# Optimization experiments

Measured on AMD Instinct MI355X. Metric: run time of the kernel, lower is better.

## Reference

```python
import jax, jax.numpy as jnp
import numpy as np

EMBED_DIM = 512
B, N = 8, 2048


def setup_inputs() -> dict:
    key = jax.random.key(0)
    ks = jax.random.split(key, 9)
    d = EMBED_DIM
    s = 1.0 / np.sqrt(d)
    return {
        "x": jax.random.normal(ks[0], (B, N, d), dtype=jnp.float32),
        "Wq": jax.random.uniform(ks[1], (d, d), jnp.float32, -s, s),
        "bq": jax.random.uniform(ks[2], (d,), jnp.float32, -s, s),
        "Wk": jax.random.uniform(ks[3], (d, d), jnp.float32, -s, s),
        "bk": jax.random.uniform(ks[4], (d,), jnp.float32, -s, s),
        "Wv": jax.random.uniform(ks[5], (d, d), jnp.float32, -s, s),
        "bv": jax.random.uniform(ks[6], (d,), jnp.float32, -s, s),
        "Wo": jax.random.uniform(ks[7], (d, d), jnp.float32, -s, s),
        "bo": jax.random.uniform(ks[8], (d,), jnp.float32, -s, s),
    }


def reference(x, Wq, bq, Wk, bk, Wv, bv, Wo, bo):
    d = x.shape[-1]
    scale = d ** (-0.5)
    q = x @ Wq + bq              # [B, N, D]
    k = x @ Wk + bk
    v = x @ Wv + bv
    attn = jnp.einsum('bnd,bmd->bnm', q, k) * scale  # [B, N, N]
    attn = jax.nn.softmax(attn, axis=-1)
    out = jnp.einsum('bnm,bmd->bnd', attn, v)
    return out @ Wo + bo
```

## Files before the change

kernel.cpp:

```cpp
#include <hip/hip_runtime.h>
#include <hip/hip_bf16.h>
#include <hip/hip_fp8.h>
#include <stdint.h>

typedef __bf16 bf16;
typedef __attribute__((ext_vector_type(8))) short short8;
typedef __attribute__((ext_vector_type(4))) float f32x4;
typedef __attribute__((ext_vector_type(4))) bf16 bf16x4;
typedef __attribute__((ext_vector_type(8))) int int8v;
typedef __attribute__((ext_vector_type(4))) int int4v;

#define DIM 512
#define NBATCH 8
#define SEQ 2048

#define VMCNT(N) asm volatile("s_waitcnt vmcnt(" #N ")" ::: "memory")
#define LGKMCNT0 asm volatile("s_waitcnt lgkmcnt(0)" ::: "memory")
#define CFENCE   asm volatile("" ::: "memory")

__device__ __forceinline__ void gld_lds16(const void* g, void* l) {
    __builtin_amdgcn_global_load_lds(
        (const __attribute__((address_space(1))) void*)g,
        (__attribute__((address_space(3))) void*)l,
        16, 0, 0);
}

__device__ __forceinline__ unsigned char f32_to_e4m3(float v) {
#if __has_builtin(__builtin_amdgcn_cvt_pk_fp8_f32)
    return (unsigned char)(__builtin_amdgcn_cvt_pk_fp8_f32(v, v, 0, false) & 0xff);
#else
    return __hip_cvt_float_to_fp8(v, __HIP_SATFINITE, __HIP_E4M3);
#endif
}

template <int MODE, int SWIZ>
__global__ __launch_bounds__(256) void gemm_bt(
    const bf16* __restrict__ A, const bf16* __restrict__ Bt,
    void* __restrict__ Cv, uint8_t* __restrict__ Vt,
    const float* __restrict__ bias, int N, int K, int gx)
{
    __shared__ bf16 smem[32768];
    bf16* Asb = smem;
    bf16* Bsb = smem + 16384;

    int bx, by;
    {
        const unsigned g = blockIdx.x;
        const unsigned xcd = g & 7;
        const unsigned t = g >> 3;
        const unsigned per = (gridDim.x >> 3) / (unsigned)gx;
        by = xcd * per + t / (unsigned)gx;
        bx = t % (unsigned)gx;
    }

    const int tid  = threadIdx.x;
    const int lane = tid & 63;
    const int w    = tid >> 6;
    const int wr   = w >> 1;
    const int wc   = w & 1;
    const int lm   = lane & 15;
    const int lk   = lane >> 4;
    const int fs   = lm & 7;
    const int rq   = tid >> 3;
    const int pc   = tid & 7;
    const int scol = ((pc ^ (rq & 7)) * 8);

    const bf16* Ag = A + (size_t)(by * 128) * K;
    const bf16* Bg = Bt + (size_t)(bx * 128) * K;

    f32x4 acc[4][4];
#pragma unroll
    for (int i = 0; i < 4; ++i)
#pragma unroll
        for (int j = 0; j < 4; ++j)
            acc[i][j] = (f32x4){0.f, 0.f, 0.f, 0.f};

    auto stage = [&](int kb, int buf) {
#pragma unroll
        for (int t = 0; t < 4; ++t) {
            const int r = t * 32 + rq;
            gld_lds16(Ag + (size_t)r * K + kb + scol,
                      Asb + buf * 8192 + t * 2048 + tid * 8);
            gld_lds16(Bg + (size_t)r * K + kb + scol,
                      Bsb + buf * 8192 + t * 2048 + tid * 8);
        }
    };
    auto compute = [&](int buf) {
        const bf16* Ab = Asb + buf * 8192;
        const bf16* Bb = Bsb + buf * 8192;
#pragma unroll
        for (int s = 0; s < 2; ++s) {
            const int u = ((s * 4 + lk) ^ fs) * 8;
            short8 fa[4], fb[4];
#pragma unroll
            for (int i = 0; i < 4; ++i)
                fa[i] = *(const short8*)&Ab[(wr * 64 + i * 16 + lm) * 64 + u];
#pragma unroll
            for (int j = 0; j < 4; ++j)
                fb[j] = *(const short8*)&Bb[(wc * 64 + j * 16 + lm) * 64 + u];
#pragma unroll
            for (int i = 0; i < 4; ++i)
#pragma unroll
                for (int j = 0; j < 4; ++j)
                    acc[i][j] = __builtin_amdgcn_mfma_f32_16x16x32_bf16(
                        fa[i], fb[j], acc[i][j], 0, 0, 0);
        }
    };

    stage(0, 0);
    const int E = K >> 6;
#pragma unroll 2
    for (int e = 0; e < E; ++e) {
        const int p = e & 1;
        CFENCE;
        __builtin_amdgcn_s_barrier();
        CFENCE;
        if (e + 1 < E) { stage((e + 1) << 6, p ^ 1); VMCNT(8); }
        else           { VMCNT(0); }
        CFENCE;
        __builtin_amdgcn_s_barrier();
        CFENCE;
        __builtin_amdgcn_s_setprio(1);
        compute(p);
        __builtin_amdgcn_s_setprio(0);
    }
    __syncthreads();

#pragma unroll
    for (int i = 0; i < 4; ++i)
#pragma unroll
        for (int j = 0; j < 4; ++j) {
            const int col = bx * 128 + wc * 64 + j * 16 + lm;
            const float bv = bias[col];
#pragma unroll
            for (int r = 0; r < 4; ++r)
                acc[i][j][r] += bv;
        }

    if (MODE == 2) {
        float* ft = (float*)smem;
        float* outp = (float*)Cv;
#pragma unroll
        for (int h = 0; h < 2; ++h) {
            if (wr == h) {
#pragma unroll
                for (int i = 0; i < 4; ++i)
#pragma unroll
                    for (int j = 0; j < 4; ++j)
#pragma unroll
                        for (int r = 0; r < 4; ++r)
                            ft[(i * 16 + lk * 4 + r) * 132 + wc * 64 + j * 16 + lm] =
                                acc[i][j][r];
            }
            __syncthreads();
            const int rr = tid >> 5, cc = (tid & 31) * 4;
#pragma unroll
            for (int p = 0; p < 8; ++p) {
                const int row = p * 8 + rr;
                *(float4*)&outp[(size_t)(by * 128 + h * 64 + row) * N +
                                bx * 128 + cc] = *(const float4*)&ft[row * 132 + cc];
            }
            __syncthreads();
        }
        return;
    }

    const int sub  = (bx * 128) >> 9;
    const int col0 = (bx * 128) & 511;

    if (sub == 2) {
        const int b  = (by * 128) >> 11;
        const int n0 = (by * 128) & 2047;
        uint8_t* t8 = (uint8_t*)smem;
#pragma unroll
        for (int i = 0; i < 4; ++i)
#pragma unroll
            for (int j = 0; j < 4; ++j)
#pragma unroll
                for (int r = 0; r < 4; ++r) {
                    const int fl = wc * 64 + j * 16 + lm;
                    const int nl = wr * 64 + i * 16 + lk * 4 + r;
                    t8[fl * 144 + nl] = f32_to_e4m3(32.0f * acc[i][j][r]);
                }
        __syncthreads();
        const int f = tid >> 1, nh = (tid & 1) * 64;
#pragma unroll
        for (int p = 0; p < 4; ++p) {
            const uint4 raw = *(const uint4*)&t8[f * 144 + nh + p * 16];
            *(uint4*)&Vt[((size_t)(b * 512 + col0 + f)) * 2048 +
                         n0 + nh + p * 16] = raw;
        }
        return;
    }

    uint8_t* d8 = (uint8_t*)Cv + (size_t)sub * 8388608;
    uint8_t* t8 = (uint8_t*)smem;
#pragma unroll
    for (int h = 0; h < 2; ++h) {
        if (wr == h) {
#pragma unroll
            for (int i = 0; i < 4; ++i)
#pragma unroll
                for (int j = 0; j < 4; ++j)
#pragma unroll
                    for (int r = 0; r < 4; ++r)
                        t8[(i * 16 + lk * 4 + r) * 144 + wc * 64 + j * 16 + lm] =
                            f32_to_e4m3(32.0f * acc[i][j][r]);
        }
        __syncthreads();
        const int rr = tid >> 3, cc = (tid & 7) * 16;
#pragma unroll
        for (int p = 0; p < 2; ++p) {
            const int row = p * 32 + rr;
            const uint4 raw = *(const uint4*)&t8[row * 144 + cc];
            *(uint4*)&d8[(size_t)(by * 128 + h * 64 + row) * 512 + col0 + cc] =
                raw;
        }
        __syncthreads();
    }
}

template <int MODE, int E>
__global__ __launch_bounds__(256) void gemm_mx(
    const uint8_t* __restrict__ A, const uint8_t* __restrict__ Bt,
    void* __restrict__ Cv, float* __restrict__ rsum,
    int N, int K, long long sA, long long sB, long long sC, float alpha,
    int gx)
{
    __shared__ uint8_t smem[49152];
    uint8_t* Ab  = smem;
    uint8_t* Bsb = smem + 16384;

    int bx, by, bz;
    {
        const unsigned g = blockIdx.x;
        bz = g & 7;
        const unsigned r = g >> 3;
        bx = r % (unsigned)gx;
        by = r / (unsigned)gx;
    }

    const int tid  = threadIdx.x;
    const int lane = tid & 63;
    const int w    = tid >> 6;
    const int wr   = w >> 1;
    const int wc   = w & 1;
    const int lm   = lane & 15;
    const int lk   = lane >> 4;
    const int rq   = tid >> 3;
    const int pc   = tid & 7;
    const int ssrc = (pc ^ (rq & 7)) * 16;
    const int ca   = ((2 * lk) ^ (lm & 7)) * 16;
    const int cb   = ((2 * lk + 1) ^ (lm & 7)) * 16;

    const size_t z = bz;
    const uint8_t* Ag = A + z * (size_t)sA + (size_t)(by * 128) * K;
    const uint8_t* Bg = Bt + z * (size_t)sB + (size_t)(bx * 128) * K;

    f32x4 acc[4][4];
#pragma unroll
    for (int i = 0; i < 4; ++i)
#pragma unroll
        for (int j = 0; j < 4; ++j)
            acc[i][j] = (f32x4){0.f, 0.f, 0.f, 0.f};

    auto stageA = [&](int kb) {
#pragma unroll
        for (int t = 0; t < 4; ++t) {
            const int r = t * 32 + rq;
            gld_lds16(Ag + (size_t)r * K + kb + ssrc,
                      Ab + t * 4096 + tid * 16);
        }
    };
    auto stageB = [&](int kb, int buf) {
#pragma unroll
        for (int t = 0; t < 4; ++t) {
            const int r = t * 32 + rq;
            gld_lds16(Bg + (size_t)r * K + kb + ssrc,
                      Bsb + buf * 16384 + t * 4096 + tid * 16);
        }
    };

    stageA(0); stageB(0, 0);

#pragma unroll
    for (int e = 0; e < E; ++e) {
        const int p = e & 1;
        VMCNT(0);
        __builtin_amdgcn_s_barrier();
        CFENCE;
        int8v fa[4];
#pragma unroll
        for (int i = 0; i < 4; ++i) {
            const uint8_t* rp = Ab + (wr * 64 + i * 16 + lm) * 128;
            const int4v lo = *(const int4v*)(rp + ca);
            const int4v hi = *(const int4v*)(rp + cb);
            fa[i] = (int8v){lo[0], lo[1], lo[2], lo[3],
                            hi[0], hi[1], hi[2], hi[3]};
        }
        LGKMCNT0;
        __builtin_amdgcn_sched_barrier(0);
        __builtin_amdgcn_s_barrier();
        CFENCE;
        if (e + 1 < E) { stageA((e + 1) * 128); stageB((e + 1) * 128, p ^ 1); }
        const uint8_t* Bs = Bsb + p * 16384;
        __builtin_amdgcn_s_setprio(1);
#pragma unroll
        for (int j = 0; j < 4; ++j) {
            const uint8_t* rp = Bs + (wc * 64 + j * 16 + lm) * 128;
            const int4v lo = *(const int4v*)(rp + ca);
            const int4v hi = *(const int4v*)(rp + cb);
            const int8v fb = (int8v){lo[0], lo[1], lo[2], lo[3],
                                     hi[0], hi[1], hi[2], hi[3]};
#pragma unroll
            for (int i = 0; i < 4; ++i)
                acc[i][j] = __builtin_amdgcn_mfma_scale_f32_16x16x128_f8f6f4(
                    fa[i], fb, acc[i][j], 0, 0, 0, 127, 0, 127);
        }
        __builtin_amdgcn_s_setprio(0);
    }
    __syncthreads();

    const int orow0 = by * 128 + wr * 64;

    if (MODE == 4) {
#pragma unroll
        for (int i = 0; i < 4; ++i) {
            float psum[4] = {0.f, 0.f, 0.f, 0.f};
#pragma unroll
            for (int j = 0; j < 4; ++j)
#pragma unroll
                for (int r = 0; r < 4; ++r) {
                    const float e = __expf(acc[i][j][r] * alpha);
                    acc[i][j][r] = e;
                    psum[r] += e;
                }
#pragma unroll
            for (int m = 1; m < 16; m <<= 1)
#pragma unroll
                for (int r = 0; r < 4; ++r) psum[r] += __shfl_xor(psum[r], m);
            if (lm == 0) {
#pragma unroll
                for (int r = 0; r < 4; ++r)
                    atomicAdd(&rsum[z * SEQ + orow0 + i * 16 + lk * 4 + r],
                              psum[r]);
            }
        }
        uint8_t* dst = (uint8_t*)Cv + z * (size_t)sC;
#pragma unroll
        for (int h = 0; h < 2; ++h) {
            if (wr == h) {
#pragma unroll
                for (int i = 0; i < 4; ++i)
#pragma unroll
                    for (int j = 0; j < 4; ++j)
#pragma unroll
                        for (int r = 0; r < 4; ++r)
                            smem[(i * 16 + lk * 4 + r) * 144 +
                                 wc * 64 + j * 16 + lm] =
                                f32_to_e4m3(acc[i][j][r]);
            }
            __syncthreads();
            const int rr = tid >> 3, cc = (tid & 7) * 16;
#pragma unroll
            for (int p = 0; p < 2; ++p) {
                const int row = p * 32 + rr;
                const uint4 raw = *(const uint4*)&smem[row * 144 + cc];
                *(uint4*)&dst[(size_t)(by * 128 + h * 64 + row) * N +
                              bx * 128 + cc] = raw;
            }
            __syncthreads();
        }
        return;
    }

#pragma unroll
    for (int i = 0; i < 4; ++i) {
        float inv[4];
#pragma unroll
        for (int r = 0; r < 4; ++r)
            inv[r] = 1.0f / (32.0f * rsum[z * SEQ + orow0 + i * 16 + lk * 4 + r]);
#pragma unroll
        for (int j = 0; j < 4; ++j)
#pragma unroll
            for (int r = 0; r < 4; ++r)
                acc[i][j][r] *= inv[r];
    }
    bf16* dst = (bf16*)Cv + z * (size_t)sC;
    bf16* tile = (bf16*)smem;
#pragma unroll
    for (int h = 0; h < 2; ++h) {
        if (wr == h) {
#pragma unroll
            for (int i = 0; i < 4; ++i)
#pragma unroll
                for (int j = 0; j < 4; ++j)
#pragma unroll
                    for (int r = 0; r < 4; ++r)
                        tile[(i * 16 + lk * 4 + r) * 136 + wc * 64 + j * 16 + lm] =
                            (bf16)acc[i][j][r];
        }
        __syncthreads();
        const int rr0 = tid >> 4, cc = (tid & 15) * 8;
#pragma unroll
        for (int p = 0; p < 4; ++p) {
            const int row = p * 16 + rr0;
            const uint4 raw = *(const uint4*)&tile[row * 136 + cc];
            *(uint4*)&dst[(size_t)(by * 128 + h * 64 + row) * N + bx * 128 + cc] =
                raw;
        }
        __syncthreads();
    }
}

__global__ __launch_bounds__(256) void cvt_f32_bf16(
    const float* __restrict__ x, bf16* __restrict__ o, int n4)
{
    const int i = blockIdx.x * 256 + threadIdx.x;
    if (i >= n4) return;
    const float4 v = ((const float4*)x)[i];
    bf16x4 b;
    b[0] = (bf16)v.x; b[1] = (bf16)v.y; b[2] = (bf16)v.z; b[3] = (bf16)v.w;
    ((bf16x4*)o)[i] = b;
}

__global__ __launch_bounds__(256) void transpose4(
    const float* __restrict__ Wq, const float* __restrict__ Wk,
    const float* __restrict__ Wv, const float* __restrict__ Wo,
    bf16* __restrict__ Wcat, bf16* __restrict__ Wto,
    const float* __restrict__ bq, const float* __restrict__ bk,
    const float* __restrict__ bv, float* __restrict__ bcat,
    float* __restrict__ rowsum)
{
    const int widx = blockIdx.z;
    const int t0 = threadIdx.x;
    if (widx == 4) {
        const int idx = (blockIdx.y * 8 + blockIdx.x) * 256 + t0;
        rowsum[idx] = 0.0f;
        if (idx < 1536)
            bcat[idx] = (idx < 512) ? bq[idx]
                      : (idx < 1024) ? bk[idx - 512] : bv[idx - 1024];
        return;
    }
    __shared__ bf16 tile[64][65];
    const float* W = (widx == 0) ? Wq : (widx == 1) ? Wk : (widx == 2) ? Wv : Wo;
    bf16* dst = (widx < 3) ? (Wcat + (size_t)widx * 512 * 512) : Wto;
    const int tx = blockIdx.x, ty = blockIdx.y;
#pragma unroll
    for (int it = 0; it < 16; ++it) {
        const int e = it * 256 + t0;
        const int r = e >> 6, c = e & 63;
        tile[r][c] = (bf16)W[(size_t)(ty * 64 + r) * 512 + tx * 64 + c];
    }
    __syncthreads();
#pragma unroll
    for (int it = 0; it < 16; ++it) {
        const int e = it * 256 + t0;
        const int o = e >> 6, i = e & 63;
        dst[(size_t)(tx * 64 + o) * 512 + ty * 64 + i] = tile[i][o];
    }
}

extern "C" void kernel_launch(void* const* d_in, const int* in_sizes, int n_in,
                              void* d_out, int out_size, void* d_ws, size_t ws_size,
                              hipStream_t stream)
{
    const float* x  = (const float*)d_in[0];
    const float* Wq = (const float*)d_in[1];
    const float* bq = (const float*)d_in[2];
    const float* Wk = (const float*)d_in[3];
    const float* bk = (const float*)d_in[4];
    const float* Wv = (const float*)d_in[5];
    const float* bv = (const float*)d_in[6];
    const float* Wo = (const float*)d_in[7];
    const float* bo = (const float*)d_in[8];
    float* out = (float*)d_out;

    char* ws = (char*)d_ws;
    bf16*    Xb     = (bf16*)(ws);
    bf16*    Ctx    = (bf16*)(ws);
    bf16*    Wcat   = (bf16*)(ws + 16777216);
    bf16*    Wto    = (bf16*)(ws + 18350080);
    float*   bcat   = (float*)(ws + 18874368);
    float*   rowsum = (float*)(ws + 18880512);
    uint8_t* Q8     = (uint8_t*)(ws + 20971520);
    uint8_t* K8     = (uint8_t*)(ws + 29360128);
    uint8_t* Vt8    = (uint8_t*)(ws + 54525952);
    uint8_t* S8     = (uint8_t*)(ws + 62914560);

    transpose4<<<dim3(8, 8, 5), 256, 0, stream>>>(
        Wq, Wk, Wv, Wo, Wcat, Wto, bq, bk, bv, bcat, rowsum);
    cvt_f32_bf16<<<8192, 256, 0, stream>>>(x, Xb, 2097152);

    const float scale = 0.044194173824159216f;

    gemm_bt<3, 2><<<1536, 256, 0, stream>>>(
        Xb, Wcat, Q8, Vt8, bcat, 1536, 512, 12);

    gemm_mx<4, 4><<<2048, 256, 0, stream>>>(
        Q8, K8, S8, rowsum, 2048, 512,
        2048LL * 512, 2048LL * 512, 2048LL * 2048, scale / 1024.0f, 16);

    gemm_mx<5, 16><<<512, 256, 0, stream>>>(
        S8, Vt8, Ctx, rowsum, 512, 2048,
        2048LL * 2048, 512LL * 2048, 2048LL * 512, 1.0f, 4);

    gemm_bt<2, 2><<<512, 256, 0, stream>>>(
        Ctx, Wto, out, nullptr, bo, 512, 512, 4);
}
```

Before: 212.6 us.

## Fuse QK^T, exp and PV into a single attention kernel

Replaces the two fp8 GEMM launches, which wrote the full exp-score matrix S8 to global memory and read it back, with one fused kernel. Each block handles 64 query rows of one batch and keeps Q in LDS. For each 128-key chunk it computes scores with MFMA, exponentiates them into an fp8 tile in LDS, then multiplies by V. Row sums are reduced per block in shared memory rather than with global atomics. The aim is to remove the large S round-trip and one launch. In exchange, K and V fragments are read straight from global memory with no staging or prefetch, and the grid has only 256 blocks, so latency hiding may be weak.

```diff
diff --git a/kernel.cpp b/kernel.cpp
--- a/kernel.cpp
+++ b/kernel.cpp
@@ -15,7 +15,6 @@
 #define SEQ 2048
 
 #define VMCNT(N) asm volatile("s_waitcnt vmcnt(" #N ")" ::: "memory")
-#define LGKMCNT0 asm volatile("s_waitcnt lgkmcnt(0)" ::: "memory")
 #define CFENCE   asm volatile("" ::: "memory")
 
 __device__ __forceinline__ void gld_lds16(const void* g, void* l) {
@@ -220,196 +219,175 @@
     }
 }
 
-template <int MODE, int E>
-__global__ __launch_bounds__(256) void gemm_mx(
-    const uint8_t* __restrict__ A, const uint8_t* __restrict__ Bt,
-    void* __restrict__ Cv, float* __restrict__ rsum,
-    int N, int K, long long sA, long long sB, long long sC, float alpha,
-    int gx)
+__global__ __launch_bounds__(256) void attn_fused(
+    const uint8_t* __restrict__ Q8, const uint8_t* __restrict__ K8,
+    const uint8_t* __restrict__ Vt8, bf16* __restrict__ Ctx, float alpha)
 {
-    __shared__ uint8_t smem[49152];
-    uint8_t* Ab  = smem;
-    uint8_t* Bsb = smem + 16384;
-
-    int bx, by, bz;
-    {
-        const unsigned g = blockIdx.x;
-        bz = g & 7;
-        const unsigned r = g >> 3;
-        bx = r % (unsigned)gx;
-        by = r / (unsigned)gx;
-    }
+    __shared__ uint8_t smem[66560];
+    uint8_t* Qs = smem;
+    uint8_t* Ss = smem + 32768;
+    float*   rs = (float*)(smem + 40960);
+
+    const unsigned g = blockIdx.x;
+    const int bz  = g & 7;
+    const int qr0 = (int)(g >> 3) * 64;
 
     const int tid  = threadIdx.x;
     const int lane = tid & 63;
     const int w    = tid >> 6;
-    const int wr   = w >> 1;
-    const int wc   = w & 1;
     const int lm   = lane & 15;
     const int lk   = lane >> 4;
-    const int rq   = tid >> 3;
-    const int pc   = tid & 7;
-    const int ssrc = (pc ^ (rq & 7)) * 16;
-    const int ca   = ((2 * lk) ^ (lm & 7)) * 16;
-    const int cb   = ((2 * lk + 1) ^ (lm & 7)) * 16;
-
-    const size_t z = bz;
-    const uint8_t* Ag = A + z * (size_t)sA + (size_t)(by * 128) * K;
-    const uint8_t* Bg = Bt + z * (size_t)sB + (size_t)(bx * 128) * K;
-
-    f32x4 acc[4][4];
-#pragma unroll
-    for (int i = 0; i < 4; ++i)
-#pragma unroll
-        for (int j = 0; j < 4; ++j)
-            acc[i][j] = (f32x4){0.f, 0.f, 0.f, 0.f};
-
-    auto stageA = [&](int kb) {
-#pragma unroll
-        for (int t = 0; t < 4; ++t) {
-            const int r = t * 32 + rq;
-            gld_lds16(Ag + (size_t)r * K + kb + ssrc,
-                      Ab + t * 4096 + tid * 16);
-        }
-    };
-    auto stageB = [&](int kb, int buf) {
-#pragma unroll
-        for (int t = 0; t < 4; ++t) {
-            const int r = t * 32 + rq;
-            gld_lds16(Bg + (size_t)r * K + kb + ssrc,
-                      Bsb + buf * 16384 + t * 4096 + tid * 16);
-        }
-    };
-
-    stageA(0); stageB(0, 0);
-
-#pragma unroll
-    for (int e = 0; e < E; ++e) {
-        const int p = e & 1;
-        VMCNT(0);
-        __builtin_amdgcn_s_barrier();
-        CFENCE;
-        int8v fa[4];
+    const int c0   = ((2 * lk) ^ (lm & 7)) * 16;
+    const int c1   = ((2 * lk + 1) ^ (lm & 7)) * 16;
+
+    {
+        const uint8_t* Qg = Q8 + (size_t)(bz * SEQ + qr0) * DIM;
+        const int R = tid >> 5;
+        const int c = tid & 31;
+        const int sc = (c ^ (R & 7)) * 16;
+#pragma unroll
+        for (int p = 0; p < 8; ++p)
+            gld_lds16(Qg + (size_t)(p * 8 + R) * DIM + sc,
+                      Qs + p * 4096 + tid * 16);
+    }
+    if (tid < 64) rs[tid] = 0.f;
+    VMCNT(0);
+    __syncthreads();
+
+    f32x4 opv[4][8];
+#pragma unroll
+    for (int i = 0; i < 4; ++i)
+#pragma unroll
+        for (int j = 0; j < 8; ++j)
+            opv[i][j] = (f32x4){0.f, 0.f, 0.f, 0.f};
+    float psum[4][4];
+#pragma unroll
+    for (int i = 0; i < 4; ++i)
+#pragma unroll
+        for (int r = 0; r < 4; ++r)
+            psum[i][r] = 0.f;
+
+    const uint8_t* Kg = K8 + (size_t)(bz * SEQ) * DIM;
+    const uint8_t* Vg = Vt8 + (size_t)(bz * DIM + w * 128) * (size_t)SEQ;
+
+    for (int kv = 0; kv < 16; ++kv) {
+        f32x4 sacc[4][2];
+#pragma unroll
+        for (int i = 0; i < 4; ++i)
+#pragma unroll
+            for (int jj = 0; jj < 2; ++jj)
+                sacc[i][jj] = (f32x4){0.f, 0.f, 0.f, 0.f};
+        const uint8_t* Kb = Kg + (size_t)(kv * 128 + w * 32) * DIM;
+#pragma unroll
+        for (int k = 0; k < 4; ++k) {
+            int8v fa[4];
+#pragma unroll
+            for (int i = 0; i < 4; ++i) {
+                const uint8_t* rp = Qs + (i * 16 + lm) * 512 + k * 128;
+                const int4v lo = *(const int4v*)(rp + c0);
+                const int4v hi = *(const int4v*)(rp + c1);
+                fa[i] = (int8v){lo[0], lo[1], lo[2], lo[3],
+                                hi[0], hi[1], hi[2], hi[3]};
+            }
+#pragma unroll
+            for (int jj = 0; jj < 2; ++jj) {
+                const uint8_t* kp = Kb + (size_t)(jj * 16 + lm) * DIM +
+                                    k * 128 + 32 * lk;
+                const int4v lo = *(const int4v*)kp;
+                const int4v hi = *(const int4v*)(kp + 16);
+                const int8v fb = (int8v){lo[0], lo[1], lo[2], lo[3],
+                                         hi[0], hi[1], hi[2], hi[3]};
+#pragma unroll
+                for (int i = 0; i < 4; ++i)
+                    sacc[i][jj] =
+                        __builtin_amdgcn_mfma_scale_f32_16x16x128_f8f6f4(
+                            fa[i], fb, sacc[i][jj], 0, 0, 0, 127, 0, 127);
+            }
+        }
+
+#pragma unroll
+        for (int i = 0; i < 4; ++i)
+#pragma unroll
+            for (int jj = 0; jj < 2; ++jj)
+#pragma unroll
+                for (int r = 0; r < 4; ++r) {
+                    const float e = __expf(sacc[i][jj][r] * alpha);
+                    psum[i][r] += e;
+                    const int m = i * 16 + lk * 4 + r;
+                    const int n = w * 32 + jj * 16 + lm;
+                    Ss[m * 128 + (((n >> 4) ^ (m & 7)) << 4) + (n & 15)] =
+                        f32_to_e4m3(e);
+                }
+
+        const uint8_t* Vb = Vg + kv * 128 + 32 * lk;
+        int8v fbv[8];
+#pragma unroll
+        for (int j = 0; j < 8; ++j) {
+            const uint8_t* vp = Vb + (size_t)(j * 16 + lm) * (size_t)SEQ;
+            const int4v lo = *(const int4v*)vp;
+            const int4v hi = *(const int4v*)(vp + 16);
+            fbv[j] = (int8v){lo[0], lo[1], lo[2], lo[3],
+                             hi[0], hi[1], hi[2], hi[3]};
+        }
+        __syncthreads();
+
+        __builtin_amdgcn_s_setprio(1);
 #pragma unroll
         for (int i = 0; i < 4; ++i) {
-            const uint8_t* rp = Ab + (wr * 64 + i * 16 + lm) * 128;
-            const int4v lo = *(const int4v*)(rp + ca);
-            const int4v hi = *(const int4v*)(rp + cb);
-            fa[i] = (int8v){lo[0], lo[1], lo[2], lo[3],
-                            hi[0], hi[1], hi[2], hi[3]};
-        }
-        LGKMCNT0;
-        __builtin_amdgcn_sched_barrier(0);
-        __builtin_amdgcn_s_barrier();
-        CFENCE;
-        if (e + 1 < E) { stageA((e + 1) * 128); stageB((e + 1) * 128, p ^ 1); }
-        const uint8_t* Bs = Bsb + p * 16384;
-        __builtin_amdgcn_s_setprio(1);
-#pragma unroll
-        for (int j = 0; j < 4; ++j) {
-            const uint8_t* rp = Bs + (wc * 64 + j * 16 + lm) * 128;
-            const int4v lo = *(const int4v*)(rp + ca);
-            const int4v hi = *(const int4v*)(rp + cb);
-            const int8v fb = (int8v){lo[0], lo[1], lo[2], lo[3],
+            const uint8_t* rp = Ss + (i * 16 + lm) * 128;
+            const int4v lo = *(const int4v*)(rp + c0);
+            const int4v hi = *(const int4v*)(rp + c1);
+            const int8v fa = (int8v){lo[0], lo[1], lo[2], lo[3],
                                      hi[0], hi[1], hi[2], hi[3]};
 #pragma unroll
-            for (int i = 0; i < 4; ++i)
-                acc[i][j] = __builtin_amdgcn_mfma_scale_f32_16x16x128_f8f6f4(
-                    fa[i], fb, acc[i][j], 0, 0, 0, 127, 0, 127);
+            for (int j = 0; j < 8; ++j)
+                opv[i][j] = __builtin_amdgcn_mfma_scale_f32_16x16x128_f8f6f4(
+                    fa, fbv[j], opv[i][j], 0, 0, 0, 127, 0, 127);
         }
         __builtin_amdgcn_s_setprio(0);
-    }
-    __syncthreads();
-
-    const int orow0 = by * 128 + wr * 64;
-
-    if (MODE == 4) {
-#pragma unroll
-        for (int i = 0; i < 4; ++i) {
-            float psum[4] = {0.f, 0.f, 0.f, 0.f};
-#pragma unroll
-            for (int j = 0; j < 4; ++j)
-#pragma unroll
-                for (int r = 0; r < 4; ++r) {
-                    const float e = __expf(acc[i][j][r] * alpha);
-                    acc[i][j][r] = e;
-                    psum[r] += e;
-                }
-#pragma unroll
-            for (int m = 1; m < 16; m <<= 1)
-#pragma unroll
-                for (int r = 0; r < 4; ++r) psum[r] += __shfl_xor(psum[r], m);
-            if (lm == 0) {
-#pragma unroll
-                for (int r = 0; r < 4; ++r)
-                    atomicAdd(&rsum[z * SEQ + orow0 + i * 16 + lk * 4 + r],
-                              psum[r]);
-            }
-        }
-        uint8_t* dst = (uint8_t*)Cv + z * (size_t)sC;
-#pragma unroll
-        for (int h = 0; h < 2; ++h) {
-            if (wr == h) {
-#pragma unroll
-                for (int i = 0; i < 4; ++i)
-#pragma unroll
-                    for (int j = 0; j < 4; ++j)
-#pragma unroll
-                        for (int r = 0; r < 4; ++r)
-                            smem[(i * 16 + lk * 4 + r) * 144 +
-                                 wc * 64 + j * 16 + lm] =
-                                f32_to_e4m3(acc[i][j][r]);
-            }
-            __syncthreads();
-            const int rr = tid >> 3, cc = (tid & 7) * 16;
-#pragma unroll
-            for (int p = 0; p < 2; ++p) {
-                const int row = p * 32 + rr;
-                const uint4 raw = *(const uint4*)&smem[row * 144 + cc];
-                *(uint4*)&dst[(size_t)(by * 128 + h * 64 + row) * N +
-                              bx * 128 + cc] = raw;
-            }
-            __syncthreads();
-        }
-        return;
-    }
-
-#pragma unroll
-    for (int i = 0; i < 4; ++i) {
-        float inv[4];
+        __syncthreads();
+    }
+
+#pragma unroll
+    for (int m = 1; m < 16; m <<= 1)
+#pragma unroll
+        for (int i = 0; i < 4; ++i)
+#pragma unroll
+            for (int r = 0; r < 4; ++r)
+                psum[i][r] += __shfl_xor(psum[i][r], m);
+    if (lm == 0) {
+#pragma unroll
+        for (int i = 0; i < 4; ++i)
+#pragma unroll
+            for (int r = 0; r < 4; ++r)
+                atomicAdd(&rs[i * 16 + lk * 4 + r], psum[i][r]);
+    }
+    __syncthreads();
+    float inv[4][4];
+#pragma unroll
+    for (int i = 0; i < 4; ++i)
 #pragma unroll
         for (int r = 0; r < 4; ++r)
-            inv[r] = 1.0f / (32.0f * rsum[z * SEQ + orow0 + i * 16 + lk * 4 + r]);
-#pragma unroll
-        for (int j = 0; j < 4; ++j)
+            inv[i][r] = 1.0f / (32.0f * rs[i * 16 + lk * 4 + r]);
+    __syncthreads();
+
+    bf16* bt = (bf16*)smem;
+#pragma unroll
+    for (int i = 0; i < 4; ++i)
+#pragma unroll
+        for (int j = 0; j < 8; ++j)
 #pragma unroll
             for (int r = 0; r < 4; ++r)
-                acc[i][j][r] *= inv[r];
-    }
-    bf16* dst = (bf16*)Cv + z * (size_t)sC;
-    bf16* tile = (bf16*)smem;
-#pragma unroll
-    for (int h = 0; h < 2; ++h) {
-        if (wr == h) {
-#pragma unroll
-            for (int i = 0; i < 4; ++i)
-#pragma unroll
-                for (int j = 0; j < 4; ++j)
-#pragma unroll
-                    for (int r = 0; r < 4; ++r)
-                        tile[(i * 16 + lk * 4 + r) * 136 + wc * 64 + j * 16 + lm] =
-                            (bf16)acc[i][j][r];
-        }
-        __syncthreads();
-        const int rr0 = tid >> 4, cc = (tid & 15) * 8;
-#pragma unroll
-        for (int p = 0; p < 4; ++p) {
-            const int row = p * 16 + rr0;
-            const uint4 raw = *(const uint4*)&tile[row * 136 + cc];
-            *(uint4*)&dst[(size_t)(by * 128 + h * 64 + row) * N + bx * 128 + cc] =
-                raw;
-        }
-        __syncthreads();
+                bt[(i * 16 + lk * 4 + r) * 520 + w * 128 + j * 16 + lm] =
+                    (bf16)(opv[i][j][r] * inv[i][r]);
+    __syncthreads();
+#pragma unroll
+    for (int p = 0; p < 16; ++p) {
+        const int row = p * 4 + (tid >> 6);
+        const uint4 raw =
+            *(const uint4*)((const uint8_t*)smem + row * 1040 + (tid & 63) * 16);
+        *(uint4*)&Ctx[(size_t)(bz * SEQ + qr0 + row) * DIM + (tid & 63) * 8] =
+            raw;
     }
 }
 
@@ -486,7 +464,6 @@
     uint8_t* Q8     = (uint8_t*)(ws + 20971520);
     uint8_t* K8     = (uint8_t*)(ws + 29360128);
     uint8_t* Vt8    = (uint8_t*)(ws + 54525952);
-    uint8_t* S8     = (uint8_t*)(ws + 62914560);
 
     transpose4<<<dim3(8, 8, 5), 256, 0, stream>>>(
         Wq, Wk, Wv, Wo, Wcat, Wto, bq, bk, bv, bcat, rowsum);
@@ -497,13 +474,7 @@
     gemm_bt<3, 2><<<1536, 256, 0, stream>>>(
         Xb, Wcat, Q8, Vt8, bcat, 1536, 512, 12);
 
-    gemm_mx<4, 4><<<2048, 256, 0, stream>>>(
-        Q8, K8, S8, rowsum, 2048, 512,
-        2048LL * 512, 2048LL * 512, 2048LL * 2048, scale / 1024.0f, 16);
-
-    gemm_mx<5, 16><<<512, 256, 0, stream>>>(
-        S8, Vt8, Ctx, rowsum, 512, 2048,
-        2048LL * 2048, 512LL * 2048, 2048LL * 512, 1.0f, 4);
+    attn_fused<<<256, 256, 0, stream>>>(Q8, K8, Vt8, Ctx, scale / 1024.0f);
 
     gemm_bt<2, 2><<<512, 256, 0, stream>>>(
         Ctx, Wto, out, nullptr, bo, 512, 512, 4);
```

Measured after the change: 246.2 us. 15.8% more time.
